# Kernel optimization log

Hardware: AMD Instinct MI355X
Metric: run time of the kernel (lower is better)

Reference implementation:

```python
import jax, jax.numpy as jnp
import numpy as np


def setup_inputs() -> dict:
    key = jax.random.key(0)
    k1, k2, k3, k4 = jax.random.split(key, 4)
    B, N, dim, heads, dim_head = 4, 1025, 768, 12, 64
    inner = heads * dim_head
    x = jax.random.normal(k1, (B, N, dim), dtype=jnp.float32)
    # binary occlusion mask over the N-1 patch tokens (CLS handled inside forward)
    mask = (jax.random.uniform(k2, (B, N - 1, dim)) > 0.5).astype(jnp.float32)
    w_qkv = jax.random.normal(k3, (inner * 3, dim), dtype=jnp.float32) * 0.02
    w_out = jax.random.normal(k4, (dim, inner), dtype=jnp.float32) * 0.02
    b_out = jnp.zeros((dim,), dtype=jnp.float32)
    return {"x": x, "mask": mask, "w_qkv": w_qkv, "w_out": w_out, "b_out": b_out, "heads": heads}


def reference(x, mask, w_qkv, w_out, b_out, heads):
    B, N, dim = x.shape
    inner = w_qkv.shape[0] // 3
    d = inner // heads
    scale = d ** -0.5

    def split_heads(t):  # [B, n, h*d] -> [B, h, n, d]
        return t.reshape(B, t.shape[1], heads, d).transpose(0, 2, 1, 3)

    qkv = x @ w_qkv.T  # [B, N, 3*inner]
    q, k, v = map(split_heads, jnp.split(qkv, 3, axis=-1))

    # --- mask propagation (torch.no_grad block) ---
    mask_sg = jax.lax.stop_gradient(mask)
    qkv_m = mask_sg @ jax.lax.stop_gradient(jnp.abs(w_qkv)).T  # [B, N-1, 3*inner]

    def norm_mask(t):
        t = split_heads(t)  # [B, h, N-1, d]
        t = t / (1e-6 + jnp.max(t, axis=2, keepdims=True))
        return jnp.concatenate([jnp.ones_like(t[:, :, :1]), t], axis=2)  # [B, h, N, d]

    q_m, k_m, v_m = map(norm_mask, jnp.split(qkv_m, 3, axis=-1))
    updated = (jnp.mean(mask_sg, axis=-1, keepdims=True) > 0.0).astype(x.dtype)  # [B, N-1, 1]
    updated = jnp.concatenate([jnp.ones_like(updated[:, :1]), updated], axis=1)  # [B, N, 1]

    # --- masked attention ---
    dots = jnp.einsum('bhnd,bhmd->bhnm', q * q_m, k * k_m) * scale
    attn = jax.nn.softmax(dots, axis=-1)
    out = jnp.einsum('bhnm,bhmd->bhnd', attn, v_m * v)
    out = out.transpose(0, 2, 1, 3).reshape(B, N, inner) * updated
    out = out @ w_out.T + b_out

    # --- mask output propagation (no grad) ---
    m = jax.lax.stop_gradient(jnp.einsum('bhnm,bhmd->bhnd', attn, v_m))
    m = m.transpose(0, 2, 1, 3).reshape(B, N, inner) * updated
    m = m @ jax.lax.stop_gradient(jnp.abs(w_out)).T
    return (out, m[:, 1:])
```

## Files before the change

kernel.cpp:

```cpp
#include <hip/hip_runtime.h>
#include <cmath>

#define TPB 256

static const int NTOK  = 1025;
static const int DIM   = 768;
static const int HEADS = 12;
static const int QK3   = 2304;
static const int ROWS  = 4 * NTOK;
static const int MROWS = 4 * (NTOK - 1);
static const int MPAD  = 4224;
static const int NPAD  = 1088;
static const size_t OUT0 = (size_t)ROWS * DIM;
static const size_t APLANE = (size_t)MPAD * DIM;

static const size_t OFF_QKV16  = 0;
static const size_t OFF_QKVM16 = 4800000;
static const size_t OFF_QE     = 9600000;
static const size_t OFF_KF     = 11300000;
static const size_t OFF_VF     = 13000000;
static const size_t OFF_ABF    = 16400000;
static const size_t OFF_WQ     = 19700000;
static const size_t OFF_WO     = 21500000;
static const size_t OFF_CMAX   = 22100000;
static const size_t OFF_UPD    = 22110000;

typedef __attribute__((ext_vector_type(8))) short short8;
typedef __attribute__((ext_vector_type(4))) float f32x4;

__device__ __forceinline__ unsigned short f2bf(float f) {
    union { float f; unsigned int u; } c; c.f = f;
    unsigned int u = c.u + 0x7fffu + ((c.u >> 16) & 1u);
    return (unsigned short)(u >> 16);
}
__device__ __forceinline__ float bf2f(unsigned short u) {
    union { unsigned int u; float f; } c; c.u = (unsigned int)u << 16;
    return c.f;
}
__device__ __forceinline__ unsigned int cvtpk(float a, float b) {
    unsigned int r;
    asm("v_cvt_pk_bf16_f32 %0, %1, %2" : "=v"(r) : "v"(a), "v"(b));
    return r;
}
__device__ __forceinline__ void gl_lds16(const unsigned short* g, unsigned short* l) {
    __builtin_amdgcn_global_load_lds(
        (const __attribute__((address_space(1))) unsigned int*)g,
        (__attribute__((address_space(3))) unsigned int*)l, 16, 0, 0);
}

__global__ __launch_bounds__(TPB)
void k_cvt(const float* __restrict__ x, const float* __restrict__ mask,
           const float* __restrict__ wqkv, const float* __restrict__ wout,
           unsigned short* __restrict__ Abf, unsigned short* __restrict__ Wq,
           unsigned short* __restrict__ Wo)
{
    const int z = blockIdx.z;
    const size_t idx = ((size_t)blockIdx.x * TPB + threadIdx.x) * 8;
    unsigned short o[8] __attribute__((aligned(16)));
    if (z <= 1) {
        if (idx >= APLANE) return;
        const int row = (int)(idx / DIM);
        const int M = z ? MROWS : ROWS;
        const float* src = z ? mask : x;
        if (row < M) {
            float a[8];
            *(float4*)&a[0] = *(const float4*)(src + idx);
            *(float4*)&a[4] = *(const float4*)(src + idx + 4);
#pragma unroll
            for (int i = 0; i < 8; ++i) o[i] = f2bf(a[i]);
        } else {
#pragma unroll
            for (int i = 0; i < 8; ++i) o[i] = 0;
        }
        *(short8*)(Abf + (size_t)z * APLANE + idx) = *(short8*)o;
    } else {
        const size_t tot = (z == 2) ? (size_t)QK3 * DIM : (size_t)DIM * DIM;
        if (idx >= tot) return;
        const float* src = (z == 2) ? wqkv : wout;
        unsigned short* dst = (z == 2) ? Wq : Wo;
        float a[8];
        *(float4*)&a[0] = *(const float4*)(src + idx);
        *(float4*)&a[4] = *(const float4*)(src + idx + 4);
        unsigned short oa[8] __attribute__((aligned(16)));
#pragma unroll
        for (int i = 0; i < 8; ++i) { o[i] = f2bf(a[i]); oa[i] = f2bf(fabsf(a[i])); }
        *(short8*)(dst + idx) = *(short8*)o;
        *(short8*)(dst + tot + idx) = *(short8*)oa;
    }
}

__global__ __launch_bounds__(TPB)
void k_gemm_qkv_mfma(const unsigned short* __restrict__ Abf,
                     const unsigned short* __restrict__ Wq,
                     unsigned short* __restrict__ qkv16,
                     unsigned short* __restrict__ qkvm16,
                     float* __restrict__ cmax)
{
    const int z = blockIdx.z;
    const int rowT = blockIdx.y * 128, colT = blockIdx.x * 128;
    if (z == 1 && rowT >= MROWS) return;
    const unsigned short* A = Abf + (size_t)z * APLANE;
    const unsigned short* B = Wq + (size_t)z * QK3 * DIM;

    __shared__ unsigned short As[128 * 64];
    __shared__ unsigned short Bs[128 * 64];

    const int t = threadIdx.x;
    const int w = t >> 6, lane = t & 63, l15 = lane & 15, quad = lane >> 4;
    const int wm = (w & 1) * 64, wn = (w >> 1) * 64;
    const int sr = t >> 2, sk = (t & 3) * 8;

    f32x4 acc[4][4];
#pragma unroll
    for (int i = 0; i < 4; ++i)
#pragma unroll
        for (int j = 0; j < 4; ++j) acc[i][j] = (f32x4){0.f, 0.f, 0.f, 0.f};

    for (int k0 = 0; k0 < DIM; k0 += 64) {
        __syncthreads();
#pragma unroll
        for (int c = 0; c < 4; ++c) {
            const int gr = sr + (c & 1) * 64;
            const int gk = k0 + (c >> 1) * 32 + sk;
            gl_lds16(A + (size_t)(rowT + gr) * DIM + gk, As + c * 2048 + t * 8);
            gl_lds16(B + (size_t)(colT + gr) * DIM + gk, Bs + c * 2048 + t * 8);
        }
        __syncthreads();
        short8 fa[2][4], fb[2][4];
#pragma unroll
        for (int kk = 0; kk < 2; ++kk) {
#pragma unroll
            for (int mi = 0; mi < 4; ++mi)
                fa[kk][mi] = *(const short8*)(As + kk * 4096 + (wm + mi * 16 + l15) * 32 + quad * 8);
#pragma unroll
            for (int ni = 0; ni < 4; ++ni)
                fb[kk][ni] = *(const short8*)(Bs + kk * 4096 + (wn + ni * 16 + l15) * 32 + quad * 8);
        }
#pragma unroll
        for (int kk = 0; kk < 2; ++kk)
#pragma unroll
            for (int mi = 0; mi < 4; ++mi)
#pragma unroll
                for (int ni = 0; ni < 4; ++ni)
                    acc[mi][ni] = __builtin_amdgcn_mfma_f32_16x16x32_bf16(fa[kk][mi], fb[kk][ni], acc[mi][ni], 0, 0, 0);
    }

    float cm[4] = {0.f, 0.f, 0.f, 0.f};
#pragma unroll
    for (int mi = 0; mi < 4; ++mi)
#pragma unroll
        for (int ni = 0; ni < 4; ++ni) {
            const int col = colT + wn + ni * 16 + l15;
#pragma unroll
            for (int r = 0; r < 4; ++r) {
                const int row = rowT + wm + mi * 16 + quad * 4 + r;
                const float v = acc[mi][ni][r];
                if (z == 0) {
                    if (row < ROWS) qkv16[(size_t)row * QK3 + col] = f2bf(v);
                } else {
                    qkvm16[(size_t)row * QK3 + col] = f2bf(v);
                    cm[ni] = fmaxf(cm[ni], v);
                }
            }
        }
    if (z == 1) {
        const int bb = rowT >> 10;
#pragma unroll
        for (int ni = 0; ni < 4; ++ni) {
            float m = cm[ni];
            m = fmaxf(m, __shfl_xor(m, 16, 64));
            m = fmaxf(m, __shfl_xor(m, 32, 64));
            if (quad == 0)
                atomicMax((int*)&cmax[bb * QK3 + colT + wn + ni * 16 + l15], __float_as_int(m));
        }
    }
}

__global__ __launch_bounds__(TPB)
void k_misc(const float* __restrict__ mask, float* __restrict__ upd)
{
    const int bx = blockIdx.x;
    const int w = threadIdx.x >> 6, lane = threadIdx.x & 63;
    const int r = bx * 4 + w;
    if (r >= ROWS) return;
    const int b = r / NTOK, n = r % NTOK;
    float res = 1.f;
    if (n > 0) {
        const float* p = mask + (size_t)(b * (NTOK - 1) + (n - 1)) * DIM;
        float s = 0.f;
        for (int i = lane; i < DIM; i += 64) s += p[i];
#pragma unroll
        for (int off = 32; off > 0; off >>= 1) s += __shfl_xor(s, off, 64);
        res = (s > 0.f) ? 1.f : 0.f;
    }
    if (lane == 0) upd[r] = res;
}

__global__ __launch_bounds__(TPB)
void k_prep(const unsigned short* __restrict__ qkv16,
            const unsigned short* __restrict__ qkvm16,
            const float* __restrict__ cmax, unsigned short* __restrict__ qe,
            unsigned short* __restrict__ kfrag, unsigned short* __restrict__ vfrag)
{
    __shared__ unsigned short Vt_l[128 * 66];
    const int t = threadIdx.x;
    const int nt = blockIdx.x, h = blockIdx.y, b = blockIdx.z;
    const int bh = b * HEADS + h;
    const int nl = t >> 2, ds0 = (t & 3) * 16;
    const int n = nt * 64 + nl;
    const bool valid = n < NTOK;
    const int col0 = h * 64 + ds0;

    unsigned short q16[16] __attribute__((aligned(16))) = {0};
    unsigned short k16[16] __attribute__((aligned(16))) = {0};
    unsigned short v16[16] __attribute__((aligned(16))) = {0};
    unsigned short qm16[16] __attribute__((aligned(16)));
    unsigned short km16[16] __attribute__((aligned(16)));
    unsigned short vm16[16] __attribute__((aligned(16)));
    float cq[16], ck[16], cv[16];

    const bool useM = valid && (n > 0);
    if (valid) {
        const size_t br = (size_t)(b * NTOK + n) * QK3 + col0;
        *(short8*)&q16[0] = *(const short8*)(qkv16 + br);
        *(short8*)&q16[8] = *(const short8*)(qkv16 + br + 8);
        *(short8*)&k16[0] = *(const short8*)(qkv16 + br + 768);
        *(short8*)&k16[8] = *(const short8*)(qkv16 + br + 776);
        *(short8*)&v16[0] = *(const short8*)(qkv16 + br + 1536);
        *(short8*)&v16[8] = *(const short8*)(qkv16 + br + 1544);
    }
    if (useM) {
        const size_t mr = (size_t)(b * 1024 + (n - 1)) * QK3 + col0;
        *(short8*)&qm16[0] = *(const short8*)(qkvm16 + mr);
        *(short8*)&qm16[8] = *(const short8*)(qkvm16 + mr + 8);
        *(short8*)&km16[0] = *(const short8*)(qkvm16 + mr + 768);
        *(short8*)&km16[8] = *(const short8*)(qkvm16 + mr + 776);
        *(short8*)&vm16[0] = *(const short8*)(qkvm16 + mr + 1536);
        *(short8*)&vm16[8] = *(const short8*)(qkvm16 + mr + 1544);
        const int cb = b * QK3 + col0;
#pragma unroll
        for (int i = 0; i < 4; ++i) {
            *(float4*)&cq[i * 4] = *(const float4*)(cmax + cb + i * 4);
            *(float4*)&ck[i * 4] = *(const float4*)(cmax + cb + 768 + i * 4);
            *(float4*)&cv[i * 4] = *(const float4*)(cmax + cb + 1536 + i * 4);
        }
    }

    unsigned short oq[16] __attribute__((aligned(16)));
    unsigned short ok[16] __attribute__((aligned(16)));
#pragma unroll
    for (int idx = 0; idx < 16; ++idx) {
        const float qm = useM ? bf2f(qm16[idx]) / (1e-6f + cq[idx]) : 1.f;
        const float km = useM ? bf2f(km16[idx]) / (1e-6f + ck[idx]) : 1.f;
        const float vm = valid ? (useM ? bf2f(vm16[idx]) / (1e-6f + cv[idx]) : 1.f) : 0.f;
        oq[idx] = f2bf(bf2f(q16[idx]) * qm * 0.18033688f);
        ok[idx] = f2bf(bf2f(k16[idx]) * km);
        const int d = ds0 + idx;
        Vt_l[d * 66 + nl]        = f2bf(bf2f(v16[idx]) * vm);
        Vt_l[(64 + d) * 66 + nl] = f2bf(vm);
    }
    {
        unsigned short* qp = qe + ((size_t)bh * NPAD + n) * 64 + ds0;
        *(short8*)qp       = *(short8*)oq;
        *(short8*)(qp + 8) = *(short8*)(oq + 8);
    }
    {
        const int nc = nl >> 4, l15 = nl & 15;
        const int kk = ds0 >> 5, qb = (ds0 & 31) >> 3;
        unsigned short* kp = kfrag + (((size_t)bh * 17 + nt) * 8 + kk * 4 + nc) * 512;
        *(short8*)(kp + ((size_t)(qb * 16 + l15)) * 8)       = *(short8*)ok;
        *(short8*)(kp + ((size_t)((qb + 1) * 16 + l15)) * 8) = *(short8*)(ok + 8);
    }
    __syncthreads();
    const int c = t >> 1, nh = (t & 1) * 32;
    unsigned short ov[32] __attribute__((aligned(16)));
#pragma unroll
    for (int i = 0; i < 32; ++i) ov[i] = Vt_l[c * 66 + nh + i];
    const int c8 = c >> 4, l15v = c & 15, kkv = nh >> 5;
    unsigned short* vp = vfrag + (((size_t)bh * 17 + nt) * 16 + c8 * 2 + kkv) * 512 + (size_t)l15v * 8;
#pragma unroll
    for (int qd = 0; qd < 4; ++qd)
        *(short8*)(vp + (size_t)qd * 128) = *(short8*)(ov + qd * 8);
}

__global__ __launch_bounds__(64, 2)
void k_attn(const unsigned short* __restrict__ qe, const unsigned short* __restrict__ kfrag,
            const unsigned short* __restrict__ vfrag, const float* __restrict__ upd,
            unsigned short* __restrict__ ab2)
{
    const int flat = blockIdx.y * 33 + blockIdx.x;
    const int d2 = (flat & 7) * 198 + (flat >> 3);
    const int bh = d2 / 33, qt = d2 - bh * 33;
    const int b = bh / HEADS, h = bh - b * HEADS;
    const int lane = threadIdx.x;
    const int l15 = lane & 15, quad = lane >> 4;
    const int q0 = qt * 32;

    short8 qf[2][2];
#pragma unroll
    for (int j = 0; j < 2; ++j) {
        const unsigned short* qp = qe + ((size_t)bh * NPAD + q0 + j * 16 + l15) * 64 + (quad << 3);
        qf[j][0] = *(const short8*)qp;
        qf[j][1] = *(const short8*)(qp + 32);
    }
    const int pA = (quad & 1) * 32 + l15;
    const int pB = pA + 16;
    const bool lo32 = (lane < 32);

    const unsigned short* kb = kfrag + (size_t)bh * (17 * 8 * 512) + (size_t)lane * 8;
    const unsigned short* vb = vfrag + (size_t)bh * (17 * 16 * 512) + (size_t)lane * 8;

    short8 kf[8], vf[16];
#pragma unroll
    for (int g = 0; g < 8; ++g) kf[g] = *(const short8*)(kb + g * 512);
#pragma unroll
    for (int g = 0; g < 16; ++g) vf[g] = *(const short8*)(vb + g * 512);

    f32x4 acc[2][8];
    float lac[2] = {0.f, 0.f};
#pragma unroll
    for (int j = 0; j < 2; ++j)
#pragma unroll
        for (int g = 0; g < 8; ++g) acc[j][g] = (f32x4){0.f, 0.f, 0.f, 0.f};

    const float EC = 14.4269504f;

#pragma clang loop unroll(disable)
    for (int kt = 0; kt < 17; ++kt) {
        f32x4 s[2][4];
        __builtin_amdgcn_s_setprio(1);
#pragma unroll
        for (int nc = 0; nc < 4; ++nc) {
#pragma unroll
            for (int j = 0; j < 2; ++j) {
                f32x4 z = (f32x4){0.f, 0.f, 0.f, 0.f};
                z = __builtin_amdgcn_mfma_f32_16x16x32_bf16(kf[nc], qf[j][0], z, 0, 0, 0);
                z = __builtin_amdgcn_mfma_f32_16x16x32_bf16(kf[4 + nc], qf[j][1], z, 0, 0, 0);
                s[j][nc] = z;
            }
        }
        __builtin_amdgcn_s_setprio(0);
        if (kt < 16) {
            const unsigned short* kn = kb + (size_t)(kt + 1) * 4096;
#pragma unroll
            for (int g = 0; g < 8; ++g) kf[g] = *(const short8*)(kn + g * 512);
        }
        short8 pf[2][2];
#pragma unroll
        for (int j = 0; j < 2; ++j) {
            unsigned int dA[4], dB[4];
            float psum = 0.f, p00 = 0.f;
#pragma unroll
            for (int nc = 0; nc < 4; ++nc) {
                const float p0 = __builtin_amdgcn_exp2f(s[j][nc][0] - EC);
                const float p1 = __builtin_amdgcn_exp2f(s[j][nc][1] - EC);
                const float p2 = __builtin_amdgcn_exp2f(s[j][nc][2] - EC);
                const float p3 = __builtin_amdgcn_exp2f(s[j][nc][3] - EC);
                dA[nc] = cvtpk(p0, p1);
                dB[nc] = cvtpk(p2, p3);
                psum += (p0 + p1) + (p2 + p3);
                if (nc == 0) p00 = p0;
            }
            if (kt < 16) lac[j] += psum;
            else if (quad == 0) lac[j] += p00;
            union { int i[4]; short8 s; } u0, u1;
            {
                const int a0 = __shfl((int)dA[0], pA, 64), a1 = __shfl((int)dA[1], pA, 64);
                const int b0 = __shfl((int)dB[0], pA, 64), b1 = __shfl((int)dB[1], pA, 64);
                const int a2 = __shfl((int)dA[0], pB, 64), a3 = __shfl((int)dA[1], pB, 64);
                const int b2 = __shfl((int)dB[0], pB, 64), b3 = __shfl((int)dB[1], pB, 64);
                u0.i[0] = lo32 ? a0 : a1;
                u0.i[1] = lo32 ? b0 : b1;
                u0.i[2] = lo32 ? a2 : a3;
                u0.i[3] = lo32 ? b2 : b3;
            }
            {
                const int a0 = __shfl((int)dA[2], pA, 64), a1 = __shfl((int)dA[3], pA, 64);
                const int b0 = __shfl((int)dB[2], pA, 64), b1 = __shfl((int)dB[3], pA, 64);
                const int a2 = __shfl((int)dA[2], pB, 64), a3 = __shfl((int)dA[3], pB, 64);
                const int b2 = __shfl((int)dB[2], pB, 64), b3 = __shfl((int)dB[3], pB, 64);
                u1.i[0] = lo32 ? a0 : a1;
                u1.i[1] = lo32 ? b0 : b1;
                u1.i[2] = lo32 ? a2 : a3;
                u1.i[3] = lo32 ? b2 : b3;
            }
            pf[j][0] = u0.s;
            pf[j][1] = u1.s;
        }
        __builtin_amdgcn_s_setprio(1);
#pragma unroll
        for (int g = 0; g < 8; ++g) {
#pragma unroll
            for (int j = 0; j < 2; ++j) {
                acc[j][g] = __builtin_amdgcn_mfma_f32_16x16x32_bf16(vf[2 * g],     pf[j][0], acc[j][g], 0, 0, 0);
                acc[j][g] = __builtin_amdgcn_mfma_f32_16x16x32_bf16(vf[2 * g + 1], pf[j][1], acc[j][g], 0, 0, 0);
            }
        }
        __builtin_amdgcn_s_setprio(0);
        if (kt < 16) {
            const unsigned short* vn = vb + (size_t)(kt + 1) * 8192;
#pragma unroll
            for (int g = 0; g < 16; ++g) vf[g] = *(const short8*)(vn + g * 512);
        }
    }

#pragma unroll
    for (int j = 0; j < 2; ++j) {
        float lq = lac[j];
        lq += __shfl_xor(lq, 16, 64);
        lq += __shfl_xor(lq, 32, 64);
        const int qrow = q0 + j * 16 + l15;
        if (qrow < NTOK) {
            const size_t rg = (size_t)b * NTOK + qrow;
            const float inv = upd[rg] / lq;
#pragma unroll
            for (int g = 0; g < 8; ++g) {
                uint2 pk;
                pk.x = cvtpk(acc[j][g][0] * inv, acc[j][g][1] * inv);
                pk.y = cvtpk(acc[j][g][2] * inv, acc[j][g][3] * inv);
                const size_t addr = (size_t)(g >> 2) * APLANE + rg * DIM + h * 64 + (g & 3) * 16 + quad * 4;
                *(uint2*)(ab2 + addr) = pk;
            }
        }
    }
}

__global__ __launch_bounds__(TPB)
void k_gemm_out_mfma(const unsigned short* __restrict__ ab2,
                     const unsigned short* __restrict__ Wo,
                     const float* __restrict__ bout, float* __restrict__ dout)
{
    const int z = blockIdx.z;
    const unsigned short* A = ab2 + (size_t)z * APLANE;
    const unsigned short* B = Wo + (size_t)z * DIM * DIM;

    __shared__ unsigned short As[128 * 32];
    __shared__ unsigned short Bs[128 * 32];

    const int t = threadIdx.x;
    const int w = t >> 6, lane = t & 63, l15 = lane & 15, quad = lane >> 4;
    const int rowT = blockIdx.y * 128, colT = blockIdx.x * 128;
    const int wm = (w & 1) * 64, wn = (w >> 1) * 64;

    const int r0 = t >> 2, kc = (t & 3) * 8;
    const unsigned short* Ap = A + (size_t)(rowT + r0) * DIM + kc;
    const unsigned short* Bp = B + (size_t)(colT + r0) * DIM + kc;

    f32x4 acc[4][4];
#pragma unroll
    for (int i = 0; i < 4; ++i)
#pragma unroll
        for (int j = 0; j < 4; ++j) acc[i][j] = (f32x4){0.f, 0.f, 0.f, 0.f};

    for (int k0 = 0; k0 < DIM; k0 += 32) {
        __syncthreads();
        gl_lds16(Ap + k0,            As + t * 8);
        gl_lds16(Ap + 64 * DIM + k0, As + (t + 256) * 8);
        gl_lds16(Bp + k0,            Bs + t * 8);
        gl_lds16(Bp + 64 * DIM + k0, Bs + (t + 256) * 8);
        __syncthreads();
        short8 fa[4], fb[4];
#pragma unroll
        for (int mi = 0; mi < 4; ++mi)
            fa[mi] = *(const short8*)(As + (wm + mi * 16 + l15) * 32 + quad * 8);
#pragma unroll
        for (int ni = 0; ni < 4; ++ni)
            fb[ni] = *(const short8*)(Bs + (wn + ni * 16 + l15) * 32 + quad * 8);
#pragma unroll
        for (int mi = 0; mi < 4; ++mi)
#pragma unroll
            for (int ni = 0; ni < 4; ++ni)
                acc[mi][ni] = __builtin_amdgcn_mfma_f32_16x16x32_bf16(fa[mi], fb[ni], acc[mi][ni], 0, 0, 0);
    }
#pragma unroll
    for (int mi = 0; mi < 4; ++mi)
#pragma unroll
        for (int ni = 0; ni < 4; ++ni) {
            const int col = colT + wn + ni * 16 + l15;
            const float bb = (z == 0) ? bout[col] : 0.f;
#pragma unroll
            for (int r = 0; r < 4; ++r) {
                const int row = rowT + wm + mi * 16 + quad * 4 + r;
                if (row >= ROWS) continue;
                const int b = row / NTOK, n = row % NTOK;
                if (z == 0) {
                    dout[(size_t)row * DIM + col] = acc[mi][ni][r] + bb;
                } else if (n >= 1) {
                    dout[OUT0 + ((size_t)(b * (NTOK - 1) + (n - 1))) * DIM + col] = acc[mi][ni][r];
                }
            }
        }
}

extern "C" void kernel_launch(void* const* d_in, const int* in_sizes, int n_in,
                              void* d_out, int out_size, void* d_ws, size_t ws_size,
                              hipStream_t stream)
{
    const float* x    = (const float*)d_in[0];
    const float* mask = (const float*)d_in[1];
    const float* wqkv = (const float*)d_in[2];
    const float* wout = (const float*)d_in[3];
    const float* bout = (const float*)d_in[4];
    float* ws = (float*)d_ws;
    unsigned short* qkv16  = (unsigned short*)(ws + OFF_QKV16);
    unsigned short* qkvm16 = (unsigned short*)(ws + OFF_QKVM16);
    unsigned short* qe  = (unsigned short*)(ws + OFF_QE);
    unsigned short* kfr = (unsigned short*)(ws + OFF_KF);
    unsigned short* vfr = (unsigned short*)(ws + OFF_VF);
    unsigned short* abf = (unsigned short*)(ws + OFF_ABF);
    unsigned short* wq  = (unsigned short*)(ws + OFF_WQ);
    unsigned short* wo  = (unsigned short*)(ws + OFF_WO);
    float* cmax = ws + OFF_CMAX;
    float* upd  = ws + OFF_UPD;
    float* out  = (float*)d_out;

    hipMemsetAsync(cmax, 0, 9216 * sizeof(float), stream);
    hipLaunchKernelGGL(k_cvt,           dim3(1584, 1, 4), dim3(TPB), 0, stream, x, mask, wqkv, wout, abf, wq, wo);
    hipLaunchKernelGGL(k_gemm_qkv_mfma, dim3(18, 33, 2),  dim3(TPB), 0, stream, abf, wq, qkv16, qkvm16, cmax);
    hipLaunchKernelGGL(k_misc,          dim3(1025),       dim3(TPB), 0, stream, mask, upd);
    hipLaunchKernelGGL(k_prep,          dim3(17, 12, 4),  dim3(TPB), 0, stream, qkv16, qkvm16, cmax, qe, kfr, vfr);
    hipLaunchKernelGGL(k_attn,          dim3(33, 48),     dim3(64),  0, stream, qe, kfr, vfr, upd, abf);
    hipLaunchKernelGGL(k_gemm_out_mfma, dim3(6, 33, 2),   dim3(TPB), 0, stream, abf, wo, bout, out);
}
```

Before: 220.7 us.

## Double-buffer LDS in QKV and output GEMMs with XCD-aware block remap

Both MFMA GEMM kernels now use two LDS buffers, so the next K-tile's global-to-LDS load is issued while the current tile is being multiplied. Explicit vmcnt waits and raw barriers replace the paired __syncthreads, and setprio raises wave priority around the MFMA block. The grids are flattened to 1D and block ids are remapped so consecutive tiles land on the same XCD for better L2 locality. Doubling LDS per block may reduce occupancy, and the hand-written waitcnt counts must match the number of loads issued per stage.

```diff
diff --git a/kernel.cpp b/kernel.cpp
--- a/kernel.cpp
+++ b/kernel.cpp
@@ -96,14 +96,19 @@
                      unsigned short* __restrict__ qkvm16,
                      float* __restrict__ cmax)
 {
-    const int z = blockIdx.z;
-    const int rowT = blockIdx.y * 128, colT = blockIdx.x * 128;
+    const int bid = blockIdx.x;
+    const int xcd = bid & 7, rr = bid >> 3;
+    const int id = (xcd < 4) ? (xcd * 149 + rr) : (596 + (xcd - 4) * 148 + rr);
+    const int z = id / 594;
+    const int rem = id - z * 594;
+    const int by = rem / 18, bx = rem - by * 18;
+    const int rowT = by * 128, colT = bx * 128;
     if (z == 1 && rowT >= MROWS) return;
     const unsigned short* A = Abf + (size_t)z * APLANE;
     const unsigned short* B = Wq + (size_t)z * QK3 * DIM;
 
-    __shared__ unsigned short As[128 * 64];
-    __shared__ unsigned short Bs[128 * 64];
+    __shared__ unsigned short As[2][128 * 64];
+    __shared__ unsigned short Bs[2][128 * 64];
 
     const int t = threadIdx.x;
     const int w = t >> 6, lane = t & 63, l15 = lane & 15, quad = lane >> 4;
@@ -116,26 +121,38 @@
 #pragma unroll
         for (int j = 0; j < 4; ++j) acc[i][j] = (f32x4){0.f, 0.f, 0.f, 0.f};
 
-    for (int k0 = 0; k0 < DIM; k0 += 64) {
-        __syncthreads();
+    auto stage = [&](int buf, int k0) {
 #pragma unroll
         for (int c = 0; c < 4; ++c) {
             const int gr = sr + (c & 1) * 64;
             const int gk = k0 + (c >> 1) * 32 + sk;
-            gl_lds16(A + (size_t)(rowT + gr) * DIM + gk, As + c * 2048 + t * 8);
-            gl_lds16(B + (size_t)(colT + gr) * DIM + gk, Bs + c * 2048 + t * 8);
-        }
-        __syncthreads();
+            gl_lds16(A + (size_t)(rowT + gr) * DIM + gk, As[buf] + c * 2048 + t * 8);
+            gl_lds16(B + (size_t)(colT + gr) * DIM + gk, Bs[buf] + c * 2048 + t * 8);
+        }
+    };
+
+    stage(0, 0);
+    for (int kt = 0; kt < 12; ++kt) {
+        const int cur = kt & 1;
+        if (kt < 11) {
+            stage(cur ^ 1, (kt + 1) * 64);
+            asm volatile("s_waitcnt vmcnt(8)" ::: "memory");
+        } else {
+            asm volatile("s_waitcnt vmcnt(0)" ::: "memory");
+        }
+        __builtin_amdgcn_s_barrier();
+        __builtin_amdgcn_sched_barrier(0);
         short8 fa[2][4], fb[2][4];
 #pragma unroll
         for (int kk = 0; kk < 2; ++kk) {
 #pragma unroll
             for (int mi = 0; mi < 4; ++mi)
-                fa[kk][mi] = *(const short8*)(As + kk * 4096 + (wm + mi * 16 + l15) * 32 + quad * 8);
+                fa[kk][mi] = *(const short8*)(As[cur] + kk * 4096 + (wm + mi * 16 + l15) * 32 + quad * 8);
 #pragma unroll
             for (int ni = 0; ni < 4; ++ni)
-                fb[kk][ni] = *(const short8*)(Bs + kk * 4096 + (wn + ni * 16 + l15) * 32 + quad * 8);
-        }
+                fb[kk][ni] = *(const short8*)(Bs[cur] + kk * 4096 + (wn + ni * 16 + l15) * 32 + quad * 8);
+        }
+        __builtin_amdgcn_s_setprio(1);
 #pragma unroll
         for (int kk = 0; kk < 2; ++kk)
 #pragma unroll
@@ -143,6 +160,9 @@
 #pragma unroll
                 for (int ni = 0; ni < 4; ++ni)
                     acc[mi][ni] = __builtin_amdgcn_mfma_f32_16x16x32_bf16(fa[kk][mi], fb[kk][ni], acc[mi][ni], 0, 0, 0);
+        __builtin_amdgcn_s_setprio(0);
+        asm volatile("s_waitcnt lgkmcnt(0)" ::: "memory");
+        __builtin_amdgcn_s_barrier();
     }
 
     float cm[4] = {0.f, 0.f, 0.f, 0.f};
@@ -430,16 +450,22 @@
                      const unsigned short* __restrict__ Wo,
                      const float* __restrict__ bout, float* __restrict__ dout)
 {
-    const int z = blockIdx.z;
+    const int bid = blockIdx.x;
+    const int xcd = bid & 7, rr = bid >> 3;
+    const int id = (xcd < 4) ? (xcd * 50 + rr) : (200 + (xcd - 4) * 49 + rr);
+    const int z = id / 198;
+    const int rem = id - z * 198;
+    const int by = rem / 6, bx = rem - by * 6;
+    const int rowT = by * 128, colT = bx * 128;
+
     const unsigned short* A = ab2 + (size_t)z * APLANE;
     const unsigned short* B = Wo + (size_t)z * DIM * DIM;
 
-    __shared__ unsigned short As[128 * 32];
-    __shared__ unsigned short Bs[128 * 32];
+    __shared__ unsigned short As[2][128 * 32];
+    __shared__ unsigned short Bs[2][128 * 32];
 
     const int t = threadIdx.x;
     const int w = t >> 6, lane = t & 63, l15 = lane & 15, quad = lane >> 4;
-    const int rowT = blockIdx.y * 128, colT = blockIdx.x * 128;
     const int wm = (w & 1) * 64, wn = (w >> 1) * 64;
 
     const int r0 = t >> 2, kc = (t & 3) * 8;
@@ -452,25 +478,40 @@
 #pragma unroll
         for (int j = 0; j < 4; ++j) acc[i][j] = (f32x4){0.f, 0.f, 0.f, 0.f};
 
-    for (int k0 = 0; k0 < DIM; k0 += 32) {
-        __syncthreads();
-        gl_lds16(Ap + k0,            As + t * 8);
-        gl_lds16(Ap + 64 * DIM + k0, As + (t + 256) * 8);
-        gl_lds16(Bp + k0,            Bs + t * 8);
-        gl_lds16(Bp + 64 * DIM + k0, Bs + (t + 256) * 8);
-        __syncthreads();
+    auto stage = [&](int buf, int k0) {
+        gl_lds16(Ap + k0,            As[buf] + t * 8);
+        gl_lds16(Ap + 64 * DIM + k0, As[buf] + (t + 256) * 8);
+        gl_lds16(Bp + k0,            Bs[buf] + t * 8);
+        gl_lds16(Bp + 64 * DIM + k0, Bs[buf] + (t + 256) * 8);
+    };
+
+    stage(0, 0);
+    for (int kt = 0; kt < 24; ++kt) {
+        const int cur = kt & 1;
+        if (kt < 23) {
+            stage(cur ^ 1, (kt + 1) * 32);
+            asm volatile("s_waitcnt vmcnt(4)" ::: "memory");
+        } else {
+            asm volatile("s_waitcnt vmcnt(0)" ::: "memory");
+        }
+        __builtin_amdgcn_s_barrier();
+        __builtin_amdgcn_sched_barrier(0);
         short8 fa[4], fb[4];
 #pragma unroll
         for (int mi = 0; mi < 4; ++mi)
-            fa[mi] = *(const short8*)(As + (wm + mi * 16 + l15) * 32 + quad * 8);
+            fa[mi] = *(const short8*)(As[cur] + (wm + mi * 16 + l15) * 32 + quad * 8);
 #pragma unroll
         for (int ni = 0; ni < 4; ++ni)
-            fb[ni] = *(const short8*)(Bs + (wn + ni * 16 + l15) * 32 + quad * 8);
+            fb[ni] = *(const short8*)(Bs[cur] + (wn + ni * 16 + l15) * 32 + quad * 8);
+        __builtin_amdgcn_s_setprio(1);
 #pragma unroll
         for (int mi = 0; mi < 4; ++mi)
 #pragma unroll
             for (int ni = 0; ni < 4; ++ni)
                 acc[mi][ni] = __builtin_amdgcn_mfma_f32_16x16x32_bf16(fa[mi], fb[ni], acc[mi][ni], 0, 0, 0);
+        __builtin_amdgcn_s_setprio(0);
+        asm volatile("s_waitcnt lgkmcnt(0)" ::: "memory");
+        __builtin_amdgcn_s_barrier();
     }
 #pragma unroll
     for (int mi = 0; mi < 4; ++mi)
@@ -516,9 +557,9 @@
 
     hipMemsetAsync(cmax, 0, 9216 * sizeof(float), stream);
     hipLaunchKernelGGL(k_cvt,           dim3(1584, 1, 4), dim3(TPB), 0, stream, x, mask, wqkv, wout, abf, wq, wo);
-    hipLaunchKernelGGL(k_gemm_qkv_mfma, dim3(18, 33, 2),  dim3(TPB), 0, stream, abf, wq, qkv16, qkvm16, cmax);
+    hipLaunchKernelGGL(k_gemm_qkv_mfma, dim3(1188),       dim3(TPB), 0, stream, abf, wq, qkv16, qkvm16, cmax);
     hipLaunchKernelGGL(k_misc,          dim3(1025),       dim3(TPB), 0, stream, mask, upd);
     hipLaunchKernelGGL(k_prep,          dim3(17, 12, 4),  dim3(TPB), 0, stream, qkv16, qkvm16, cmax, qe, kfr, vfr);
     hipLaunchKernelGGL(k_attn,          dim3(33, 48),     dim3(64),  0, stream, qe, kfr, vfr, upd, abf);
-    hipLaunchKernelGGL(k_gemm_out_mfma, dim3(6, 33, 2),   dim3(TPB), 0, stream, abf, wo, bout, out);
-}
+    hipLaunchKernelGGL(k_gemm_out_mfma, dim3(396),        dim3(TPB), 0, stream, abf, wo, bout, out);
+}
```

Measured after the change: 223.3 us. About the same (+1.1%).
